# Kernel tuning notes

Hardware: AMD Instinct MI355X
Metric: run time of the kernel (lower is better)

The kernel has to match this reference:

```python
import jax, jax.numpy as jnp
import numpy as np

B, N, F_IN, T = 4, 10000, 16, 12
E = 160000
K = 3
C_CHEB = 64
C_TIME = 64
LN_EPS = 1e-5


def _lambda_max(row, col, n):
    # Power iteration on the unnormalized Laplacian L = D - A (what
    # LaplacianLambdaMax computes with normalization=None).
    deg = np.bincount(row, minlength=n).astype(np.float64)
    rng = np.random.default_rng(123)
    v = rng.standard_normal(n)
    v /= np.linalg.norm(v)
    for _ in range(100):
        agg = np.zeros(n)
        np.add.at(agg, col, v[row])
        w = deg * v - agg
        v = w / max(np.linalg.norm(w), 1e-12)
    agg = np.zeros(n)
    np.add.at(agg, col, v[row])
    return np.float32(v @ (deg * v - agg))


def setup_inputs() -> dict:
    rng = np.random.default_rng(0)
    ei = rng.integers(0, N, size=(2, E))
    lam = _lambda_max(ei[0], ei[1], N)
    key = jax.random.key(0)
    k = jax.random.split(key, 8)
    sF = 1.0 / np.sqrt(F_IN)
    sC = 1.0 / np.sqrt(3 * C_CHEB)
    return {
        "x": jax.random.normal(k[0], (B, N, F_IN, T), jnp.float32),
        "edge_index": jnp.asarray(ei, dtype=jnp.int32),
        "lambda_max": jnp.float32(lam),
        "cheb_W": jax.random.normal(k[1], (K, F_IN, C_CHEB), jnp.float32) * sF,
        "cheb_b": jax.random.normal(k[2], (C_CHEB,), jnp.float32) * 0.01,
        "time_W": jax.random.normal(k[3], (C_TIME, C_CHEB, 1, 3), jnp.float32) * sC,
        "time_b": jax.random.normal(k[4], (C_TIME,), jnp.float32) * 0.01,
        "res_W": jax.random.normal(k[5], (C_TIME, F_IN, 1, 1), jnp.float32) * sF,
        "res_b": jax.random.normal(k[6], (C_TIME,), jnp.float32) * 0.01,
        "ln_gamma": jnp.ones((C_TIME,), jnp.float32),
        "ln_beta": jnp.zeros((C_TIME,), jnp.float32),
    }


def reference(x, edge_index, lambda_max, cheb_W, cheb_b, time_W, time_b,
              res_W, res_b, ln_gamma, ln_beta):
    Bb, Nn, Fin, Tt = x.shape
    row, col = edge_index[0], edge_index[1]
    # deg from scatter of unit edge weights at row (PyG get_laplacian)
    deg = jax.ops.segment_sum(jnp.ones(row.shape[0], x.dtype), row, num_segments=Nn)

    # --- ChebConv over all (batch, time) slices jointly ---
    # (B,N,F,T) -> (N, B*T, F): node axis leading for gather/scatter
    v = jnp.transpose(x, (1, 0, 3, 2)).reshape(Nn, Bb * Tt, Fin)

    def Lhat(u):  # scaled Laplacian L_hat = 2(D - A)/lambda_max - I
        agg = jax.ops.segment_sum(u[row], col, num_segments=Nn)
        return (2.0 / lambda_max) * (deg[:, None, None] * u - agg) - u

    Tx0 = v
    out = jnp.einsum('nbf,fc->nbc', Tx0, cheb_W[0])
    Tx1 = Lhat(Tx0)
    out = out + jnp.einsum('nbf,fc->nbc', Tx1, cheb_W[1])
    for k in range(2, cheb_W.shape[0]):
        Tx2 = 2.0 * Lhat(Tx1) - Tx0
        out = out + jnp.einsum('nbf,fc->nbc', Tx2, cheb_W[k])
        Tx0, Tx1 = Tx1, Tx2
    spatial = jax.nn.relu(out + cheb_b)  # (N, B*T, C_cheb)

    # (N, B*T, C) -> (B, C, N, T) for NCHW temporal conv
    spatial = spatial.reshape(Nn, Bb, Tt, C_CHEB)
    spatial = jnp.transpose(spatial, (1, 3, 0, 2))  # (B,C,N,T)

    dn = ('NCHW', 'OIHW', 'NCHW')
    tc = jax.lax.conv_general_dilated(spatial, time_W, (1, 1), ((0, 0), (1, 1)),
                                      dimension_numbers=dn) + time_b[None, :, None, None]
    xr = jnp.transpose(x, (0, 2, 1, 3))  # (B,F,N,T)
    res = jax.lax.conv_general_dilated(xr, res_W, (1, 1), ((0, 0), (0, 0)),
                                       dimension_numbers=dn) + res_b[None, :, None, None]

    h = jax.nn.relu(res + tc)                  # (B, C_time, N, T)
    h = jnp.transpose(h, (0, 3, 2, 1))         # (B, T, N, C_time)
    mu = jnp.mean(h, axis=-1, keepdims=True)
    var = jnp.mean((h - mu) ** 2, axis=-1, keepdims=True)
    hn = (h - mu) * jax.lax.rsqrt(var + LN_EPS) * ln_gamma + ln_beta
    return jnp.transpose(hn, (0, 2, 3, 1))     # (B, N, C_time, T)
```

## Files before the change

kernel.cpp:

```cpp
#include <hip/hip_runtime.h>

typedef short bf16x8 __attribute__((ext_vector_type(8)));
typedef float f32x4 __attribute__((ext_vector_type(4)));

#define NN 10000
#define EE 160000
#define BB 4
#define TTT 12
#define FFF 16
#define CCC 64
#define BT 48
#define NF 768
#define SLOTS 64

#define TCS 72
#define SPS 80
#define HMS 68

#define WS_DEG     0u
#define WS_CNT     40960u
#define WS_CWT     81920u
#define WS_RWTB    90112u
#define WS_WKT     94208u
#define WS_CSRP    118784u
#define WS_VBF     2678784u
#define WS_TX1BF   18040320u

__device__ __forceinline__ unsigned short f2bf(float x){
    unsigned int u = __float_as_uint(x);
    u += 0x7FFFu + ((u >> 16) & 1u);
    return (unsigned short)(u >> 16);
}
__device__ __forceinline__ float bf2f(unsigned short h){
    return __uint_as_float(((unsigned int)h) << 16);
}

__global__ __launch_bounds__(256) void k_setup(
    const float* __restrict__ x, const int* __restrict__ ei,
    const float* __restrict__ chW, const float* __restrict__ tW, const float* __restrict__ rW,
    float* __restrict__ deg, int* __restrict__ csrp,
    unsigned short* __restrict__ vbf, unsigned short* __restrict__ tx1bf,
    unsigned short* __restrict__ cWt, unsigned short* __restrict__ rWtb,
    unsigned short* __restrict__ wkt)
{
    __shared__ float s[768];
    int bid = blockIdx.x, tid = threadIdx.x;
    if (bid < 625){
        int e = bid * 256 + tid;
        if (e < EE) atomicAdd(&deg[ei[e]], 1.0f);
    } else if (bid < 3125){
        csrp[(bid - 625) * 256 + tid] = NN;
    } else if (bid < 13125){
        int n = bid - 3125;
        if (tid < 192){
            int f = tid / 12, t = tid % 12;
            #pragma unroll
            for (int b = 0; b < BB; ++b)
                s[b * 192 + t * 16 + f] = x[(size_t)(b * NN + n) * 192 + tid];
        }
        __syncthreads();
        if (tid < 192){
            ushort4 w = { f2bf(s[tid * 4]), f2bf(s[tid * 4 + 1]),
                          f2bf(s[tid * 4 + 2]), f2bf(s[tid * 4 + 3]) };
            *(ushort4*)&vbf[(size_t)n * NF + tid * 4] = w;
        }
    } else if (bid == 13125){
        if (tid < 192){
            ushort4 z = { 0, 0, 0, 0 };
            *(ushort4*)&vbf[(size_t)NN * NF + tid * 4]   = z;
            *(ushort4*)&tx1bf[(size_t)NN * NF + tid * 4] = z;
        }
    } else {
        int idx = (bid - 13126) * 256 + tid;
        if (idx < 4096){
            int c = idx >> 6, k = idx & 63;
            float v = 0.f;
            if (k < 48){ int kk = k >> 4, f = k & 15; v = chW[kk * 1024 + f * 64 + c]; }
            cWt[idx] = f2bf(v);
        } else if (idx < 6144){
            int j = idx - 4096;
            int o = j >> 5, k = j & 31;
            float v = (k < 16) ? rW[o * 16 + k] : 0.f;
            rWtb[j] = f2bf(v);
        } else {
            int j = idx - 6144;
            int kk = j >> 12; int r = j & 4095;
            int o = r >> 6, dc = r & 63;
            wkt[j] = f2bf(tW[(o * 64 + dc) * 3 + kk]);
        }
    }
}

__global__ void k_fillpad(const int* __restrict__ ei, int* __restrict__ cnt,
                          int* __restrict__ csrp){
    int e = blockIdx.x * 256 + threadIdx.x;
    if (e < EE){
        int c = ei[EE + e];
        int slot = atomicAdd(&cnt[c], 1);
        if (slot < SLOTS) csrp[c * SLOTS + slot] = ei[e];
    }
}

#define GATHER8(SRC, ACC0, ACC1, ACC2, ACC3, Q)                                   \
    {                                                                             \
        ushort4 p0 = *(const ushort4*)&SRC[(size_t)e0.x * NF + (Q) * 4];          \
        ushort4 p1 = *(const ushort4*)&SRC[(size_t)e0.y * NF + (Q) * 4];          \
        ushort4 p2 = *(const ushort4*)&SRC[(size_t)e0.z * NF + (Q) * 4];          \
        ushort4 p3 = *(const ushort4*)&SRC[(size_t)e0.w * NF + (Q) * 4];          \
        ushort4 p4 = *(const ushort4*)&SRC[(size_t)e1.x * NF + (Q) * 4];          \
        ushort4 p5 = *(const ushort4*)&SRC[(size_t)e1.y * NF + (Q) * 4];          \
        ushort4 p6 = *(const ushort4*)&SRC[(size_t)e1.z * NF + (Q) * 4];          \
        ushort4 p7 = *(const ushort4*)&SRC[(size_t)e1.w * NF + (Q) * 4];          \
        ACC0 += bf2f(p0.x)+bf2f(p1.x)+bf2f(p2.x)+bf2f(p3.x)                       \
              + bf2f(p4.x)+bf2f(p5.x)+bf2f(p6.x)+bf2f(p7.x);                      \
        ACC1 += bf2f(p0.y)+bf2f(p1.y)+bf2f(p2.y)+bf2f(p3.y)                       \
              + bf2f(p4.y)+bf2f(p5.y)+bf2f(p6.y)+bf2f(p7.y);                      \
        ACC2 += bf2f(p0.z)+bf2f(p1.z)+bf2f(p2.z)+bf2f(p3.z)                       \
              + bf2f(p4.z)+bf2f(p5.z)+bf2f(p6.z)+bf2f(p7.z);                      \
        ACC3 += bf2f(p0.w)+bf2f(p1.w)+bf2f(p2.w)+bf2f(p3.w)                       \
              + bf2f(p4.w)+bf2f(p5.w)+bf2f(p6.w)+bf2f(p7.w);                      \
    }

__global__ __launch_bounds__(192) void k_lhat(
        const unsigned short* __restrict__ vbf, const float* __restrict__ deg,
        const int* __restrict__ cnt, const int* __restrict__ csrp,
        const float* __restrict__ lam, unsigned short* __restrict__ tx1bf){
    int n = blockIdx.x;
    int q = threadIdx.x;
    float s2 = 2.0f / lam[0];
    float dn = deg[n];
    int iters = (cnt[n] + 7) >> 3;
    const int4* cp = (const int4*)(csrp + n * SLOTS);
    float a0 = 0.f, a1 = 0.f, a2 = 0.f, a3 = 0.f;
    for (int it = 0; it < iters; ++it){
        int4 e0 = cp[it * 2], e1 = cp[it * 2 + 1];
        GATHER8(vbf, a0, a1, a2, a3, q);
    }
    ushort4 hv = *(const ushort4*)&vbf[(size_t)n * NF + q * 4];
    float v0 = bf2f(hv.x), v1 = bf2f(hv.y), v2 = bf2f(hv.z), v3 = bf2f(hv.w);
    ushort4 o4 = { f2bf(s2 * (dn * v0 - a0) - v0),
                   f2bf(s2 * (dn * v1 - a1) - v1),
                   f2bf(s2 * (dn * v2 - a2) - v2),
                   f2bf(s2 * (dn * v3 - a3) - v3) };
    *(ushort4*)&tx1bf[(size_t)n * NF + q * 4] = o4;
}

__global__ __launch_bounds__(256) void k_fused(
    const unsigned short* __restrict__ vbf, const unsigned short* __restrict__ tx1bf,
    const float* __restrict__ deg, const int* __restrict__ cnt, const int* __restrict__ csrp,
    const float* __restrict__ lam,
    const unsigned short* __restrict__ cWt, const float* __restrict__ chebB,
    const unsigned short* __restrict__ wkt, const float* __restrict__ timeB,
    const unsigned short* __restrict__ rWtb, const float* __restrict__ resB,
    const float* __restrict__ gamma, const float* __restrict__ beta,
    float* __restrict__ out)
{
    __shared__ unsigned short tcat[48 * TCS];
    __shared__ unsigned short spl[56 * SPS];
    __shared__ float hmat[48 * HMS];
    __shared__ float2 red[48];

    int n = blockIdx.x;
    int tid = threadIdx.x;

    {
        int rid = tid >> 5;
        int cc = tid & 31;
        int b = rid >> 1, p = (rid & 1) * 13;
        *(unsigned int*)&spl[(b * 14 + p) * SPS + cc * 2] = 0u;
    }

    if (tid < 192){
        float s2 = 2.0f / lam[0];
        float dn = deg[n];
        ushort4 hv = *(const ushort4*)&vbf[(size_t)n * NF + tid * 4];
        ushort4 hu = *(const ushort4*)&tx1bf[(size_t)n * NF + tid * 4];
        float a0 = 0.f, a1 = 0.f, a2 = 0.f, a3 = 0.f;
        int iters = (cnt[n] + 7) >> 3;
        const int4* cp = (const int4*)(csrp + n * SLOTS);
        for (int it = 0; it < iters; ++it){
            int4 e0 = cp[it * 2], e1 = cp[it * 2 + 1];
            GATHER8(tx1bf, a0, a1, a2, a3, tid);
        }
        float u0 = bf2f(hu.x), u1 = bf2f(hu.y), u2 = bf2f(hu.z), u3 = bf2f(hu.w);
        float v0 = bf2f(hv.x), v1 = bf2f(hv.y), v2 = bf2f(hv.z), v3 = bf2f(hv.w);
        ushort4 w2 = { f2bf(2.0f * (s2 * (dn * u0 - a0) - u0) - v0),
                       f2bf(2.0f * (s2 * (dn * u1 - a1) - u1) - v1),
                       f2bf(2.0f * (s2 * (dn * u2 - a2) - u2) - v2),
                       f2bf(2.0f * (s2 * (dn * u3 - a3) - u3) - v3) };
        ushort4 zz = { 0, 0, 0, 0 };
        int bt = tid >> 2, ch = tid & 3;
        *(ushort4*)&tcat[bt * TCS +      ch * 4] = hv;
        *(ushort4*)&tcat[bt * TCS + 16 + ch * 4] = hu;
        *(ushort4*)&tcat[bt * TCS + 32 + ch * 4] = w2;
        *(ushort4*)&tcat[bt * TCS + 48 + ch * 4] = zz;
    }
    __syncthreads();

    int lane = tid & 63;
    int nt   = tid >> 6;
    int ln   = lane & 15;
    int quad = lane >> 4;
    int q8   = quad * 8;
    int col  = nt * 16 + ln;

    {
        bf16x8 cb0 = *(const bf16x8*)&cWt[col * 64 + q8];
        bf16x8 cb1 = *(const bf16x8*)&cWt[col * 64 + 32 + q8];
        bf16x8 rb  = *(const bf16x8*)&rWtb[col * 32 + q8];
        f32x4 cacc[3], racc[3];
        #pragma unroll
        for (int mt = 0; mt < 3; ++mt){
            bf16x8 a0 = *(const bf16x8*)&tcat[(mt * 16 + ln) * TCS + q8];
            bf16x8 a1 = *(const bf16x8*)&tcat[(mt * 16 + ln) * TCS + 32 + q8];
            f32x4 z = {0.f, 0.f, 0.f, 0.f};
            cacc[mt] = __builtin_amdgcn_mfma_f32_16x16x32_bf16(a0, cb0, z, 0, 0, 0);
            cacc[mt] = __builtin_amdgcn_mfma_f32_16x16x32_bf16(a1, cb1, cacc[mt], 0, 0, 0);
            racc[mt] = __builtin_amdgcn_mfma_f32_16x16x32_bf16(a0, rb, z, 0, 0, 0);
        }
        float cb = chebB[col];
        #pragma unroll
        for (int mt = 0; mt < 3; ++mt){
            #pragma unroll
            for (int i = 0; i < 4; ++i){
                int r = mt * 16 + quad * 4 + i;
                int bb = (r * 43) >> 9;
                int tt = r - 12 * bb;
                float val = fmaxf(cacc[mt][i] + cb, 0.0f);
                spl[(bb * 14 + tt + 1) * SPS + col] = f2bf(val);
            }
        }
        __syncthreads();

        bf16x8 wb[3][2];
        #pragma unroll
        for (int kk = 0; kk < 3; ++kk){
            wb[kk][0] = *(const bf16x8*)&wkt[kk * 4096 + col * 64 + q8];
            wb[kk][1] = *(const bf16x8*)&wkt[kk * 4096 + col * 64 + 32 + q8];
        }
        float tb = timeB[col] + resB[col];
        #pragma unroll
        for (int mt = 0; mt < 3; ++mt){
            int bt = mt * 16 + ln;
            int bb = (bt * 43) >> 9;
            int tt = bt - 12 * bb;
            int rbase = bb * 14 + tt;
            f32x4 tacc = {0.f, 0.f, 0.f, 0.f};
            #pragma unroll
            for (int kk = 0; kk < 3; ++kk){
                bf16x8 a0 = *(const bf16x8*)&spl[(rbase + kk) * SPS + q8];
                bf16x8 a1 = *(const bf16x8*)&spl[(rbase + kk) * SPS + 32 + q8];
                tacc = __builtin_amdgcn_mfma_f32_16x16x32_bf16(a0, wb[kk][0], tacc, 0, 0, 0);
                tacc = __builtin_amdgcn_mfma_f32_16x16x32_bf16(a1, wb[kk][1], tacc, 0, 0, 0);
            }
            #pragma unroll
            for (int i = 0; i < 4; ++i){
                int r = mt * 16 + quad * 4 + i;
                float h = fmaxf(tacc[i] + racc[mt][i] + tb, 0.0f);
                hmat[r * HMS + col] = h;
            }
        }
    }
    __syncthreads();

    if (tid < 192){
        int row = tid >> 2, p = tid & 3;
        const float4* h4 = (const float4*)&hmat[row * HMS + p * 16];
        float4 A = h4[0], Bv = h4[1], Cv = h4[2], Dv = h4[3];
        float s = A.x+A.y+A.z+A.w + Bv.x+Bv.y+Bv.z+Bv.w
                + Cv.x+Cv.y+Cv.z+Cv.w + Dv.x+Dv.y+Dv.z+Dv.w;
        float q = A.x*A.x+A.y*A.y+A.z*A.z+A.w*A.w + Bv.x*Bv.x+Bv.y*Bv.y+Bv.z*Bv.z+Bv.w*Bv.w
                + Cv.x*Cv.x+Cv.y*Cv.y+Cv.z*Cv.z+Cv.w*Cv.w + Dv.x*Dv.x+Dv.y*Dv.y+Dv.z*Dv.z+Dv.w*Dv.w;
        s += __shfl_xor(s, 1); q += __shfl_xor(q, 1);
        s += __shfl_xor(s, 2); q += __shfl_xor(q, 2);
        if (p == 0) red[row] = make_float2(s, q);
    }
    __syncthreads();

    {
        int g = nt, o = lane;
        float gam = gamma[o], bet = beta[o];
        float res[12];
        #pragma unroll
        for (int t = 0; t < 12; ++t){
            int row = g * 12 + t;
            float h = hmat[row * HMS + o];
            float2 m = red[row];
            float mu  = m.x * (1.0f / 64.0f);
            float var = m.y * (1.0f / 64.0f) - mu * mu;
            float r   = rsqrtf(var + 1e-5f);
            res[t] = (h - mu) * r * gam + bet;
        }
        size_t obase = ((size_t)(g * NN + n) * CCC + o) * TTT;
        float4* op = (float4*)(out + obase);
        op[0] = make_float4(res[0], res[1], res[2],  res[3]);
        op[1] = make_float4(res[4], res[5], res[6],  res[7]);
        op[2] = make_float4(res[8], res[9], res[10], res[11]);
    }
}

extern "C" void kernel_launch(void* const* d_in, const int* in_sizes, int n_in,
                              void* d_out, int out_size, void* d_ws, size_t ws_size,
                              hipStream_t stream)
{
    (void)in_sizes; (void)n_in; (void)out_size; (void)ws_size;
    const float* x   = (const float*)d_in[0];
    const int*   ei  = (const int*)  d_in[1];
    const float* lam = (const float*)d_in[2];
    const float* chW = (const float*)d_in[3];
    const float* chB = (const float*)d_in[4];
    const float* tW  = (const float*)d_in[5];
    const float* tB  = (const float*)d_in[6];
    const float* rW  = (const float*)d_in[7];
    const float* rB  = (const float*)d_in[8];
    const float* gam = (const float*)d_in[9];
    const float* bet = (const float*)d_in[10];
    float* out = (float*)d_out;

    char* ws = (char*)d_ws;
    float* deg  = (float*)(ws + WS_DEG);
    int*   cnt  = (int*)  (ws + WS_CNT);
    unsigned short* cWt  = (unsigned short*)(ws + WS_CWT);
    unsigned short* rWtb = (unsigned short*)(ws + WS_RWTB);
    unsigned short* wkt  = (unsigned short*)(ws + WS_WKT);
    int*   csrp = (int*)  (ws + WS_CSRP);
    unsigned short* vbf   = (unsigned short*)(ws + WS_VBF);
    unsigned short* tx1bf = (unsigned short*)(ws + WS_TX1BF);

    hipMemsetAsync(ws, 0, 81920, stream);
    k_setup  <<<13198, 256, 0, stream>>>(x, ei, chW, tW, rW, deg, csrp,
                                         vbf, tx1bf, cWt, rWtb, wkt);
    k_fillpad<<<625, 256, 0, stream>>>(ei, cnt, csrp);
    k_lhat   <<<NN, 192, 0, stream>>>(vbf, deg, cnt, csrp, lam, tx1bf);
    k_fused  <<<NN, 256, 0, stream>>>(vbf, tx1bf, deg, cnt, csrp, lam,
                                      cWt, chB, wkt, tB, rWtb, rB, gam, bet, out);
}
```

Baseline: 285.1 us.

## Merge CSR fill into setup kernel, memset padding, unroll gather, alias LDS buffers

The separate k_fillpad launch is folded into k_setup. The CSR padding is now written by a byte memset (0x7F) and neighbour indices are clamped to NN at use, so the sentinel still hits the zero row. The x-to-bf16 transpose now uses one thread per output vector without shared memory, which shrinks the setup grid. k_lhat gathers 16 neighbours per iteration, and k_fused aliases its shared buffers into one smaller region with a tighter SPS stride, aiming for higher occupancy. The risks are the extra clamp instructions, the strided uncoalesced reads of x, and correctness of the LDS aliasing.

```diff
diff --git a/kernel.cpp b/kernel.cpp
--- a/kernel.cpp
+++ b/kernel.cpp
@@ -14,7 +14,7 @@
 #define SLOTS 64
 
 #define TCS 72
-#define SPS 80
+#define SPS 72
 #define HMS 68
 
 #define WS_DEG     0u
@@ -35,43 +35,70 @@
     return __uint_as_float(((unsigned int)h) << 16);
 }
 
+#define GMIN4(E)                                                                  \
+    E.x = E.x < NN ? E.x : NN; E.y = E.y < NN ? E.y : NN;                         \
+    E.z = E.z < NN ? E.z : NN; E.w = E.w < NN ? E.w : NN;
+
+#define GATHER8(SRC, EA, EB, ACC0, ACC1, ACC2, ACC3, Q)                           \
+    {                                                                             \
+        ushort4 p0 = *(const ushort4*)&SRC[(size_t)EA.x * NF + (Q) * 4];          \
+        ushort4 p1 = *(const ushort4*)&SRC[(size_t)EA.y * NF + (Q) * 4];          \
+        ushort4 p2 = *(const ushort4*)&SRC[(size_t)EA.z * NF + (Q) * 4];          \
+        ushort4 p3 = *(const ushort4*)&SRC[(size_t)EA.w * NF + (Q) * 4];          \
+        ushort4 p4 = *(const ushort4*)&SRC[(size_t)EB.x * NF + (Q) * 4];          \
+        ushort4 p5 = *(const ushort4*)&SRC[(size_t)EB.y * NF + (Q) * 4];          \
+        ushort4 p6 = *(const ushort4*)&SRC[(size_t)EB.z * NF + (Q) * 4];          \
+        ushort4 p7 = *(const ushort4*)&SRC[(size_t)EB.w * NF + (Q) * 4];          \
+        ACC0 += bf2f(p0.x)+bf2f(p1.x)+bf2f(p2.x)+bf2f(p3.x)                       \
+              + bf2f(p4.x)+bf2f(p5.x)+bf2f(p6.x)+bf2f(p7.x);                      \
+        ACC1 += bf2f(p0.y)+bf2f(p1.y)+bf2f(p2.y)+bf2f(p3.y)                       \
+              + bf2f(p4.y)+bf2f(p5.y)+bf2f(p6.y)+bf2f(p7.y);                      \
+        ACC2 += bf2f(p0.z)+bf2f(p1.z)+bf2f(p2.z)+bf2f(p3.z)                       \
+              + bf2f(p4.z)+bf2f(p5.z)+bf2f(p6.z)+bf2f(p7.z);                      \
+        ACC3 += bf2f(p0.w)+bf2f(p1.w)+bf2f(p2.w)+bf2f(p3.w)                       \
+              + bf2f(p4.w)+bf2f(p5.w)+bf2f(p6.w)+bf2f(p7.w);                      \
+    }
+
 __global__ __launch_bounds__(256) void k_setup(
     const float* __restrict__ x, const int* __restrict__ ei,
     const float* __restrict__ chW, const float* __restrict__ tW, const float* __restrict__ rW,
-    float* __restrict__ deg, int* __restrict__ csrp,
+    float* __restrict__ deg, int* __restrict__ cnt, int* __restrict__ csrp,
     unsigned short* __restrict__ vbf, unsigned short* __restrict__ tx1bf,
     unsigned short* __restrict__ cWt, unsigned short* __restrict__ rWtb,
     unsigned short* __restrict__ wkt)
 {
-    __shared__ float s[768];
     int bid = blockIdx.x, tid = threadIdx.x;
     if (bid < 625){
         int e = bid * 256 + tid;
         if (e < EE) atomicAdd(&deg[ei[e]], 1.0f);
+    } else if (bid < 1250){
+        int e = (bid - 625) * 256 + tid;
+        if (e < EE){
+            int c = ei[EE + e];
+            int slot = atomicAdd(&cnt[c], 1);
+            if (slot < SLOTS) csrp[c * SLOTS + slot] = ei[e];
+        }
     } else if (bid < 3125){
-        csrp[(bid - 625) * 256 + tid] = NN;
-    } else if (bid < 13125){
-        int n = bid - 3125;
-        if (tid < 192){
-            int f = tid / 12, t = tid % 12;
-            #pragma unroll
-            for (int b = 0; b < BB; ++b)
-                s[b * 192 + t * 16 + f] = x[(size_t)(b * NN + n) * 192 + tid];
-        }
-        __syncthreads();
-        if (tid < 192){
-            ushort4 w = { f2bf(s[tid * 4]), f2bf(s[tid * 4 + 1]),
-                          f2bf(s[tid * 4 + 2]), f2bf(s[tid * 4 + 3]) };
-            *(ushort4*)&vbf[(size_t)n * NF + tid * 4] = w;
-        }
-    } else if (bid == 13125){
+        int u = (bid - 1250) * 256 + tid;
+        int n = u / 48, r = u - n * 48;
+        int t = r >> 2, j = r & 3;
+        #pragma unroll
+        for (int b = 0; b < BB; ++b){
+            const float* xp = x + (size_t)(b * NN + n) * 192;
+            ushort4 w = { f2bf(xp[(4 * j + 0) * 12 + t]),
+                          f2bf(xp[(4 * j + 1) * 12 + t]),
+                          f2bf(xp[(4 * j + 2) * 12 + t]),
+                          f2bf(xp[(4 * j + 3) * 12 + t]) };
+            *(ushort4*)&vbf[(size_t)n * NF + b * 192 + t * 16 + j * 4] = w;
+        }
+    } else if (bid == 3125){
         if (tid < 192){
             ushort4 z = { 0, 0, 0, 0 };
             *(ushort4*)&vbf[(size_t)NN * NF + tid * 4]   = z;
             *(ushort4*)&tx1bf[(size_t)NN * NF + tid * 4] = z;
         }
     } else {
-        int idx = (bid - 13126) * 256 + tid;
+        int idx = (bid - 3126) * 256 + tid;
         if (idx < 4096){
             int c = idx >> 6, k = idx & 63;
             float v = 0.f;
@@ -84,42 +111,12 @@
             rWtb[j] = f2bf(v);
         } else {
             int j = idx - 6144;
-            int kk = j >> 12; int r = j & 4095;
-            int o = r >> 6, dc = r & 63;
+            int kk = j >> 12; int r2 = j & 4095;
+            int o = r2 >> 6, dc = r2 & 63;
             wkt[j] = f2bf(tW[(o * 64 + dc) * 3 + kk]);
         }
     }
 }
-
-__global__ void k_fillpad(const int* __restrict__ ei, int* __restrict__ cnt,
-                          int* __restrict__ csrp){
-    int e = blockIdx.x * 256 + threadIdx.x;
-    if (e < EE){
-        int c = ei[EE + e];
-        int slot = atomicAdd(&cnt[c], 1);
-        if (slot < SLOTS) csrp[c * SLOTS + slot] = ei[e];
-    }
-}
-
-#define GATHER8(SRC, ACC0, ACC1, ACC2, ACC3, Q)                                   \
-    {                                                                             \
-        ushort4 p0 = *(const ushort4*)&SRC[(size_t)e0.x * NF + (Q) * 4];          \
-        ushort4 p1 = *(const ushort4*)&SRC[(size_t)e0.y * NF + (Q) * 4];          \
-        ushort4 p2 = *(const ushort4*)&SRC[(size_t)e0.z * NF + (Q) * 4];          \
-        ushort4 p3 = *(const ushort4*)&SRC[(size_t)e0.w * NF + (Q) * 4];          \
-        ushort4 p4 = *(const ushort4*)&SRC[(size_t)e1.x * NF + (Q) * 4];          \
-        ushort4 p5 = *(const ushort4*)&SRC[(size_t)e1.y * NF + (Q) * 4];          \
-        ushort4 p6 = *(const ushort4*)&SRC[(size_t)e1.z * NF + (Q) * 4];          \
-        ushort4 p7 = *(const ushort4*)&SRC[(size_t)e1.w * NF + (Q) * 4];          \
-        ACC0 += bf2f(p0.x)+bf2f(p1.x)+bf2f(p2.x)+bf2f(p3.x)                       \
-              + bf2f(p4.x)+bf2f(p5.x)+bf2f(p6.x)+bf2f(p7.x);                      \
-        ACC1 += bf2f(p0.y)+bf2f(p1.y)+bf2f(p2.y)+bf2f(p3.y)                       \
-              + bf2f(p4.y)+bf2f(p5.y)+bf2f(p6.y)+bf2f(p7.y);                      \
-        ACC2 += bf2f(p0.z)+bf2f(p1.z)+bf2f(p2.z)+bf2f(p3.z)                       \
-              + bf2f(p4.z)+bf2f(p5.z)+bf2f(p6.z)+bf2f(p7.z);                      \
-        ACC3 += bf2f(p0.w)+bf2f(p1.w)+bf2f(p2.w)+bf2f(p3.w)                       \
-              + bf2f(p4.w)+bf2f(p5.w)+bf2f(p6.w)+bf2f(p7.w);                      \
-    }
 
 __global__ __launch_bounds__(192) void k_lhat(
         const unsigned short* __restrict__ vbf, const float* __restrict__ deg,
@@ -129,12 +126,16 @@
     int q = threadIdx.x;
     float s2 = 2.0f / lam[0];
     float dn = deg[n];
-    int iters = (cnt[n] + 7) >> 3;
+    int c = cnt[n]; c = c > SLOTS ? SLOTS : c;
+    int iters = (c + 15) >> 4;
     const int4* cp = (const int4*)(csrp + n * SLOTS);
     float a0 = 0.f, a1 = 0.f, a2 = 0.f, a3 = 0.f;
     for (int it = 0; it < iters; ++it){
-        int4 e0 = cp[it * 2], e1 = cp[it * 2 + 1];
-        GATHER8(vbf, a0, a1, a2, a3, q);
+        int4 e0 = cp[it * 4], e1 = cp[it * 4 + 1];
+        int4 e2 = cp[it * 4 + 2], e3 = cp[it * 4 + 3];
+        GMIN4(e0) GMIN4(e1) GMIN4(e2) GMIN4(e3)
+        GATHER8(vbf, e0, e1, a0, a1, a2, a3, q);
+        GATHER8(vbf, e2, e3, a0, a1, a2, a3, q);
     }
     ushort4 hv = *(const ushort4*)&vbf[(size_t)n * NF + q * 4];
     float v0 = bf2f(hv.x), v1 = bf2f(hv.y), v2 = bf2f(hv.z), v3 = bf2f(hv.w);
@@ -155,10 +156,11 @@
     const float* __restrict__ gamma, const float* __restrict__ beta,
     float* __restrict__ out)
 {
-    __shared__ unsigned short tcat[48 * TCS];
-    __shared__ unsigned short spl[56 * SPS];
-    __shared__ float hmat[48 * HMS];
-    __shared__ float2 red[48];
+    __shared__ __align__(16) char smem[21120];
+    unsigned short* spl  = (unsigned short*)smem;
+    float2*         red  = (float2*)smem;
+    unsigned short* tcat = (unsigned short*)(smem + 8064);
+    float*          hmat = (float*)(smem + 8064);
 
     int n = blockIdx.x;
     int tid = threadIdx.x;
@@ -176,11 +178,13 @@
         ushort4 hv = *(const ushort4*)&vbf[(size_t)n * NF + tid * 4];
         ushort4 hu = *(const ushort4*)&tx1bf[(size_t)n * NF + tid * 4];
         float a0 = 0.f, a1 = 0.f, a2 = 0.f, a3 = 0.f;
-        int iters = (cnt[n] + 7) >> 3;
+        int c = cnt[n]; c = c > SLOTS ? SLOTS : c;
+        int iters = (c + 7) >> 3;
         const int4* cp = (const int4*)(csrp + n * SLOTS);
         for (int it = 0; it < iters; ++it){
             int4 e0 = cp[it * 2], e1 = cp[it * 2 + 1];
-            GATHER8(tx1bf, a0, a1, a2, a3, tid);
+            GMIN4(e0) GMIN4(e1)
+            GATHER8(tx1bf, e0, e1, a0, a1, a2, a3, tid);
         }
         float u0 = bf2f(hu.x), u1 = bf2f(hu.y), u2 = bf2f(hu.z), u3 = bf2f(hu.w);
         float v0 = bf2f(hv.x), v1 = bf2f(hv.y), v2 = bf2f(hv.z), v3 = bf2f(hv.w);
@@ -328,9 +332,9 @@
     unsigned short* tx1bf = (unsigned short*)(ws + WS_TX1BF);
 
     hipMemsetAsync(ws, 0, 81920, stream);
-    k_setup  <<<13198, 256, 0, stream>>>(x, ei, chW, tW, rW, deg, csrp,
-                                         vbf, tx1bf, cWt, rWtb, wkt);
-    k_fillpad<<<625, 256, 0, stream>>>(ei, cnt, csrp);
+    hipMemsetAsync(ws + WS_CSRP, 0x7F, NN * SLOTS * 4, stream);
+    k_setup  <<<3198, 256, 0, stream>>>(x, ei, chW, tW, rW, deg, cnt, csrp,
+                                        vbf, tx1bf, cWt, rWtb, wkt);
     k_lhat   <<<NN, 192, 0, stream>>>(vbf, deg, cnt, csrp, lam, tx1bf);
     k_fused  <<<NN, 256, 0, stream>>>(vbf, tx1bf, deg, cnt, csrp, lam,
                                       cWt, chB, wkt, tB, rWtb, rB, gam, bet, out);
```

Result: no change. 281.3 us (-1.3%).
